# Performance work log

Measured on AMD Instinct MI355X. Metric: run time of the kernel, lower is better.

## Reference

```python
import jax, jax.numpy as jnp
import numpy as np

B, N = 4, 8192
DIM, HEADS = 512, 8
DH = DIM // HEADS
DT, DELTA, FF = 128, 64, 4 * DIM


def _lin(key, fan_in, fan_out):
    # torch nn.Linear default init: U(-1/sqrt(fan_in), 1/sqrt(fan_in))
    s = 1.0 / np.sqrt(fan_in)
    k1, k2 = jax.random.split(key)
    w = jax.random.uniform(k1, (fan_in, fan_out), minval=-s, maxval=s, dtype=jnp.float32)
    b = jax.random.uniform(k2, (fan_out,), minval=-s, maxval=s, dtype=jnp.float32)
    return w, b


def setup_inputs() -> dict:
    key = jax.random.key(0)
    ks = jax.random.split(key, 16)
    inp = {}
    inp['node_features'] = jax.random.normal(ks[0], (B, N, DIM), dtype=jnp.float32)
    inp['diffusion_time'] = jax.random.normal(ks[1], (B, DT), dtype=jnp.float32)
    inp['positions'] = jax.random.normal(ks[2], (B, N, 2), dtype=jnp.float32)
    inp['node_mask'] = jnp.ones((B, N), dtype=jnp.float32)
    inp['yy_w'], inp['yy_b'] = _lin(ks[3], DT, DT)
    inp['pos1_w'], inp['pos1_b'] = _lin(ks[4], 2, 64)
    inp['pos2_w'], inp['pos2_b'] = _lin(ks[5], 64, DELTA)
    inp['linx_w'], inp['linx_b'] = _lin(ks[6], DIM, DIM)
    inp['cat_w'], inp['cat_b'] = _lin(ks[7], DIM + DELTA + DT, DIM)
    inp['ln1_g'] = jnp.ones((DIM,), jnp.float32)
    inp['ln1_b'] = jnp.zeros((DIM,), jnp.float32)
    inp['q_w'] = _lin(ks[8], DIM, DIM)[0]  # no bias
    inp['k_w'] = _lin(ks[9], DIM, DIM)[0]
    inp['v_w'] = _lin(ks[10], DIM, DIM)[0]
    inp['attn_out_w'], inp['attn_out_b'] = _lin(ks[11], DIM, DIM)
    inp['ln2_g'] = jnp.ones((DIM,), jnp.float32)
    inp['ln2_b'] = jnp.zeros((DIM,), jnp.float32)
    inp['ff1_w'], inp['ff1_b'] = _lin(ks[12], DIM, FF)
    inp['ff2_w'], inp['ff2_b'] = _lin(ks[13], FF, DIM)
    inp['head2pos_w'], inp['head2pos_b'] = _lin(ks[14], DIM, 2)
    return inp


def _layernorm(x, g, b, eps=1e-5):
    mu = jnp.mean(x, axis=-1, keepdims=True)
    var = jnp.mean(jnp.square(x - mu), axis=-1, keepdims=True)
    return (x - mu) * jax.lax.rsqrt(var + eps) * g + b


def reference(node_features, diffusion_time, positions, node_mask,
              yy_w, yy_b, pos1_w, pos1_b, pos2_w, pos2_b,
              linx_w, linx_b, cat_w, cat_b,
              ln1_g, ln1_b, q_w, k_w, v_w, attn_out_w, attn_out_b,
              ln2_g, ln2_b, ff1_w, ff1_b, ff2_w, ff2_b,
              head2pos_w, head2pos_b):
    b, n, _ = node_features.shape
    mask = node_mask[..., None]  # (b, n, 1)

    # transform_diffusion_time (not last layer): y = y_y(diffusion_time)
    y = diffusion_time @ yy_w + yy_b  # (b, dy)

    # transform_positions_for_attention
    p = positions * mask
    pnorm = jnp.linalg.norm(p, axis=-1, keepdims=True)
    p_unit = p / (pnorm + 1e-7)
    delta = jax.nn.relu(p_unit @ pos1_w + pos1_b) @ pos2_w + pos2_b  # (b, n, delta)

    # feature concat + projection
    tx = node_features @ linx_w + linx_b  # (b, n, dim)
    t = jnp.broadcast_to(y[:, None, :], (b, n, y.shape[-1]))
    cat = jnp.concatenate([tx, delta, t], axis=-1) @ cat_w + cat_b  # (b, n, dim)

    # LinearAttentionTransformer, depth=1, non-causal global linear attention
    # block 1: x = x + attn(LN(x))
    h = _layernorm(cat, ln1_g, ln1_b)
    q = (h @ q_w).reshape(b, n, HEADS, DH).transpose(0, 2, 1, 3)  # (b, h, n, d)
    k = (h @ k_w).reshape(b, n, HEADS, DH).transpose(0, 2, 1, 3)
    v = (h @ v_w).reshape(b, n, HEADS, DH).transpose(0, 2, 1, 3)
    q = jax.nn.softmax(q, axis=-1) * (DH ** -0.5)  # softmax over feature dim
    k = jax.nn.softmax(k, axis=2)                   # softmax over sequence dim
    context = jnp.einsum('bhnd,bhne->bhde', k, v)   # (b, h, d, d)
    attn = jnp.einsum('bhnd,bhde->bhne', q, context)  # (b, h, n, d)
    attn = attn.transpose(0, 2, 1, 3).reshape(b, n, DIM)
    x = cat + (attn @ attn_out_w + attn_out_b)

    # block 2: x = x + ff(LN(x)), GELU feedforward
    h2 = _layernorm(x, ln2_g, ln2_b)
    x = x + (jax.nn.gelu(h2 @ ff1_w + ff1_b) @ ff2_w + ff2_b)

    # head_features_to_position
    pos_out = x @ head2pos_w + head2pos_b  # (b, n, 2)
    return (x, y, pos_out)
```

## Files before the change

### kernel.cpp

```cpp
#include <hip/hip_runtime.h>
#include <hip/hip_bf16.h>
#include <math.h>

#define NB 4
#define NN 8192
#define ROWS (NB*NN)
#define DIMC 512
#define HEADS 8
#define DT 128
#define DELTA 64
#define FF 2048
#define KCATP 640

#define OFF_R0     ((size_t)0)
#define OFF_CAW    ((size_t)8388608)
#define OFF_R1     ((size_t)10485760)
#define OFF_R2     ((size_t)18874368)
#define OFF_CATWT  ((size_t)27262976)
#define OFF_KVT    ((size_t)27426816)
#define OFF_QWT    ((size_t)27688960)
#define OFF_F1WT   ((size_t)27820032)
#define OFF_F2WT   ((size_t)28344320)
#define OFF_LXWB   ((size_t)28868608)
#define OFF_CW0T   ((size_t)28999680)
#define OFF_Y      ((size_t)29130752)
#define OFF_BB     ((size_t)29131264)
#define OFF_PM     ((size_t)29133312)
#define OFF_PS     ((size_t)29264384)
#define OFF_M      ((size_t)29395456)
#define OFF_SINV   ((size_t)29397504)
#define OFF_CTX    ((size_t)29399552)

typedef __attribute__((ext_vector_type(8))) short bf16x8;
typedef __attribute__((ext_vector_type(4))) float f32x4;
typedef __attribute__((ext_vector_type(8))) unsigned short us8;

static __device__ __forceinline__ unsigned short f2b(float x) {
    __hip_bfloat16 h = __float2bfloat16(x);
    return __builtin_bit_cast(unsigned short, h);
}
static __device__ __forceinline__ float b2f(unsigned short u) {
    return __bfloat162float(__builtin_bit_cast(__hip_bfloat16, u));
}
static __device__ __forceinline__ float gelu_tanh(float x) {
    float z2 = 1.5957691216057308f * (x + 0.044715f * x * x * x);
    float t = __expf(z2);
    return x - x / (t + 1.0f);
}

#define GLOAD16(g, l) __builtin_amdgcn_global_load_lds( \
    (const __attribute__((address_space(1))) void*)(g), \
    (__attribute__((address_space(3))) void*)(l), 16, 0, 0)

__global__ void y_kernel(const float* __restrict__ dt, const float* __restrict__ yyw,
                         const float* __restrict__ yyb, float* __restrict__ y_ws,
                         float* __restrict__ y_out) {
    int idx = blockIdx.x * 128 + threadIdx.x;
    int b = idx >> 7, j = idx & 127;
    float acc = yyb[j];
    for (int c = 0; c < DT; ++c) acc += dt[b * DT + c] * yyw[c * DT + j];
    y_ws[idx] = acc;
    y_out[idx] = acc;
}

__global__ void bb_kernel(const float* __restrict__ linxb, const float* __restrict__ catw,
                          const float* __restrict__ catb, const float* __restrict__ y,
                          float* __restrict__ bb) {
    int idx = blockIdx.x * 256 + threadIdx.x;
    int b = idx >> 9, n = idx & 511;
    float acc = catb[n];
    for (int c = 0; c < DIMC; ++c) acc += linxb[c] * catw[(size_t)c * DIMC + n];
    const float* cw3 = catw + (size_t)(DIMC + DELTA) * DIMC;
    for (int j = 0; j < DT; ++j) acc += y[b * DT + j] * cw3[(size_t)j * DIMC + n];
    bb[idx] = acc;
}

__global__ __launch_bounds__(256) void delta_kernel(
    const float* __restrict__ pos, const float* __restrict__ mask,
    const float* __restrict__ w1, const float* __restrict__ b1,
    const float* __restrict__ w2, const float* __restrict__ b2,
    unsigned short* __restrict__ catA) {
    int lane = threadIdx.x & 63;
    size_t row = (size_t)blockIdx.x * 4 + (threadIdx.x >> 6);
    float mk = mask[row];
    float px = pos[row * 2] * mk, py = pos[row * 2 + 1] * mk;
    float nrm = sqrtf(px * px + py * py) + 1e-7f;
    float ux = px / nrm, uy = py / nrm;
    float t1 = fmaxf(ux * w1[lane] + uy * w1[64 + lane] + b1[lane], 0.0f);
    float acc = b2[lane];
    #pragma unroll
    for (int j = 0; j < 64; ++j) {
        float tv = __shfl(t1, j, 64);
        acc += tv * w2[j * 64 + lane];
    }
    catA[row * KCATP + DIMC + lane] = f2b(acc);
    catA[row * KCATP + 576 + lane] = 0;
}

__global__ void zcat_kernel(unsigned short* __restrict__ catWT) {
    int idx = blockIdx.x * 256 + threadIdx.x;
    int n = idx >> 6, c = 576 + (idx & 63);
    catWT[(size_t)n * KCATP + c] = 0;
}

__global__ void conv_bf16(const float* __restrict__ in, unsigned short* __restrict__ out, int n8) {
    int i = blockIdx.x * 256 + threadIdx.x;
    if (i >= n8) return;
    const float* p = in + (size_t)i * 8;
    us8 o;
    #pragma unroll
    for (int j = 0; j < 8; ++j) o[j] = f2b(p[j]);
    *(us8*)(out + (size_t)i * 8) = o;
}

__global__ void conv_bf16_strided(const float* __restrict__ in, unsigned short* __restrict__ out,
                                  int ldo) {
    int i = blockIdx.x * 256 + threadIdx.x;
    int row = i >> 6, c8 = (i & 63) * 8;
    const float* p = in + (size_t)row * DIMC + c8;
    us8 o;
    #pragma unroll
    for (int j = 0; j < 8; ++j) o[j] = f2b(p[j]);
    *(us8*)(out + (size_t)row * ldo + c8) = o;
}

__global__ __launch_bounds__(256) void transconv(const float* __restrict__ in,
                                                 unsigned short* __restrict__ out,
                                                 int R, int C, int ldo) {
    __shared__ float tile[32][33];
    int bx = blockIdx.x * 32;
    int by = blockIdx.y * 32;
    int tx = threadIdx.x & 31, ty = threadIdx.x >> 5;
    #pragma unroll
    for (int i = 0; i < 4; ++i) {
        int r = ty + i * 8;
        tile[r][tx] = in[(size_t)(by + r) * C + bx + tx];
    }
    __syncthreads();
    #pragma unroll
    for (int i = 0; i < 4; ++i) {
        int r = ty + i * 8;
        out[(size_t)(bx + r) * ldo + by + tx] = f2b(tile[tx][r]);
    }
}

__global__ __launch_bounds__(128) void ln_kernel(
    const float* __restrict__ src, unsigned short* __restrict__ dst,
    const float* __restrict__ g, const float* __restrict__ bta) {
    size_t row = blockIdx.x;
    int t = threadIdx.x;
    const float* s = src + row * DIMC;
    float4 x = *(const float4*)(s + t * 4);
    float sum = x.x + x.y + x.z + x.w;
    float sq = x.x * x.x + x.y * x.y + x.z * x.z + x.w * x.w;
    #pragma unroll
    for (int o = 32; o; o >>= 1) { sum += __shfl_down(sum, o, 64); sq += __shfl_down(sq, o, 64); }
    __shared__ float sh[4];
    if ((t & 63) == 0) { sh[(t >> 6) * 2] = sum; sh[(t >> 6) * 2 + 1] = sq; }
    __syncthreads();
    sum = sh[0] + sh[2]; sq = sh[1] + sh[3];
    float mean = sum * (1.0f / DIMC);
    float var = sq * (1.0f / DIMC) - mean * mean;
    float rstd = rsqrtf(fmaxf(var, 0.0f) + 1e-5f);
    float4 gv = *(const float4*)(g + t * 4);
    float4 bv = *(const float4*)(bta + t * 4);
    ushort4 ov;
    ov.x = f2b((x.x - mean) * rstd * gv.x + bv.x);
    ov.y = f2b((x.y - mean) * rstd * gv.y + bv.y);
    ov.z = f2b((x.z - mean) * rstd * gv.z + bv.z);
    ov.w = f2b((x.w - mean) * rstd * gv.w + bv.w);
    *(ushort4*)(dst + row * DIMC + t * 4) = ov;
}

template <int EPI, int SWZ>
__global__ __launch_bounds__(512, 4) void gemm256(
    const unsigned short* __restrict__ A, int lda,
    const unsigned short* __restrict__ Bt, int ldb,
    const float* __restrict__ bias,
    const float* __restrict__ extra, int batch_rows,
    void* __restrict__ Cv, void* __restrict__ Cv2,
    int M, int N, int K,
    size_t b_stride, int rows_per_batch) {
    extern __shared__ char lds[];
    const int tid = threadIdx.x;
    const int lane = tid & 63, wv = tid >> 6;
    const int wr = wv >> 1, wc = wv & 1;
    const int lr = lane & 15, lch = lane >> 4;

    int bxi = blockIdx.x, byi = blockIdx.y;
    if constexpr (SWZ) {
        int l = byi * gridDim.x + bxi;
        int xcd = l & 7, j = l >> 3;
        byi = xcd * (gridDim.y >> 3) + j / gridDim.x;
        bxi = j % gridDim.x;
    }
    const int bm = byi * 256, bn = bxi * 128;

    const unsigned short* Bb = Bt;
    if (rows_per_batch) Bb = Bt + (size_t)(bm / rows_per_batch) * b_stride;

    const int srow = tid >> 2;
    const int schunk = tid & 3;

    auto stage = [&](int s, int kcol) {
        char* dstA = lds + (size_t)s * 24576;
        #pragma unroll
        for (int i = 0; i < 2; ++i) {
            int row = srow + 128 * i;
            int gc = schunk ^ ((row >> 1) & 3);
            GLOAD16((const char*)(A + (size_t)(bm + row) * lda + kcol) + gc * 16,
                    dstA + (size_t)(tid + 512 * i) * 16);
        }
        char* dstB = lds + (size_t)s * 24576 + 16384;
        {
            int row = srow;
            int gc = schunk ^ ((row >> 1) & 3);
            GLOAD16((const char*)(Bb + (size_t)(bn + row) * ldb + kcol) + gc * 16,
                    dstB + (size_t)tid * 16);
        }
    };

    f32x4 acc[4][4] = {};
    const int nt = K >> 5;

    stage(0, 0);
    stage(1, 32);
    __builtin_amdgcn_sched_barrier(0);
    asm volatile("s_waitcnt vmcnt(3)" ::: "memory");
    __builtin_amdgcn_sched_barrier(0);
    __builtin_amdgcn_s_barrier();

    int slot = 0;
    for (int t = 0; t < nt; ++t) {
        const char* base = lds + (size_t)slot * 24576;
        bf16x8 afr[4], bfr[4];
        #pragma unroll
        for (int n = 0; n < 4; ++n) {
            int bc = wc * 64 + n * 16 + lr;
            bfr[n] = *(const bf16x8*)(base + 16384 + bc * 64 + ((lch ^ ((bc >> 1) & 3)) << 4));
        }
        #pragma unroll
        for (int m = 0; m < 4; ++m) {
            int ar = wr * 64 + m * 16 + lr;
            afr[m] = *(const bf16x8*)(base + ar * 64 + ((lch ^ ((ar >> 1) & 3)) << 4));
        }
        const bool pf2 = (t + 2 < nt);
        if (pf2) {
            int s2 = slot >= 1 ? slot - 1 : 2;
            stage(s2, (t + 2) << 5);
        }
        __builtin_amdgcn_sched_barrier(0);
        asm volatile("s_waitcnt lgkmcnt(0)" ::: "memory");
        __builtin_amdgcn_sched_barrier(0);
        __builtin_amdgcn_s_setprio(1);
        #pragma unroll
        for (int m = 0; m < 4; ++m)
            #pragma unroll
            for (int n = 0; n < 4; ++n)
                acc[m][n] = __builtin_amdgcn_mfma_f32_16x16x32_bf16(
                    afr[m], bfr[n], acc[m][n], 0, 0, 0);
        __builtin_amdgcn_s_setprio(0);
        if (t + 1 < nt) {
            if (pf2) asm volatile("s_waitcnt vmcnt(3)" ::: "memory");
            else     asm volatile("s_waitcnt vmcnt(0)" ::: "memory");
            __builtin_amdgcn_sched_barrier(0);
        }
        __builtin_amdgcn_s_barrier();
        slot = slot < 2 ? slot + 1 : 0;
    }

    const int g4 = lch * 4;
    if constexpr (EPI == 7) {
        #pragma unroll
        for (int m = 0; m < 4; ++m)
            #pragma unroll
            for (int r = 0; r < 4; ++r) {
                float v0 = acc[m][0][r], v1 = acc[m][1][r];
                float v2 = acc[m][2][r], v3 = acc[m][3][r];
                float mx = fmaxf(fmaxf(v0, v1), fmaxf(v2, v3));
                #pragma unroll
                for (int o = 1; o < 16; o <<= 1) mx = fmaxf(mx, __shfl_xor(mx, o, 64));
                float e0 = __expf(v0 - mx), e1 = __expf(v1 - mx);
                float e2 = __expf(v2 - mx), e3 = __expf(v3 - mx);
                float s = e0 + e1 + e2 + e3;
                #pragma unroll
                for (int o = 1; o < 16; o <<= 1) s += __shfl_xor(s, o, 64);
                float sc = 0.125f / s;
                int rr = bm + wr * 64 + m * 16 + g4 + r;
                unsigned short* dst = (unsigned short*)Cv + (size_t)rr * N + bn + wc * 64 + lr;
                dst[0]  = f2b(e0 * sc);
                dst[16] = f2b(e1 * sc);
                dst[32] = f2b(e2 * sc);
                dst[48] = f2b(e3 * sc);
            }
    } else {
        #pragma unroll
        for (int m = 0; m < 4; ++m)
            #pragma unroll
            for (int n = 0; n < 4; ++n) {
                int col = bn + wc * 64 + n * 16 + lr;
                #pragma unroll
                for (int r = 0; r < 4; ++r) {
                    int rr = bm + wr * 64 + m * 16 + g4 + r;
                    float v = acc[m][n][r];
                    if (EPI == 1) {
                        ((unsigned short*)Cv)[(size_t)rr * N + col] = f2b(gelu_tanh(v + bias[col]));
                    } else if (EPI == 2) {
                        ((float*)Cv)[(size_t)rr * N + col] += v + bias[col];
                    } else if (EPI == 3) {
                        ((float*)Cv)[(size_t)rr * N + col] = v + extra[(size_t)(rr / batch_rows) * N + col];
                    } else if (EPI == 6) {
                        unsigned short* dst = (col >> 9) ? (unsigned short*)Cv2 : (unsigned short*)Cv;
                        dst[(size_t)rr * 512 + (col & 511)] = f2b(v);
                    }
                }
            }
    }
}

#define BM 128
#define BN 128
#define BK 64

template <int EPI>
__global__ __launch_bounds__(256) void gemm_mfma(
    const unsigned short* __restrict__ A, int lda,
    const unsigned short* __restrict__ Bt, int ldb,
    void* __restrict__ Cv, int M, int N, int K, int ldo) {
    __shared__ unsigned short As[2][BM * BK];
    __shared__ unsigned short Bs[2][BN * BK];
    int bm = blockIdx.y * BM, bn = blockIdx.x * BN;
    int tid = threadIdx.x;
    int lane = tid & 63, wv = tid >> 6;
    int wr = (wv >> 1) * 64, wc = (wv & 1) * 64;
    int g16 = (lane >> 4) << 4;
    int lr = lane & 15;
    int sw = (lr & 7) << 4;

    int srow = tid >> 3;
    int skb = (tid & 7) * 16;
    int sxor = skb ^ ((srow & 7) << 4);

    auto stage = [&](int buf, int k0) {
        #pragma unroll
        for (int i = 0; i < 4; ++i) {
            int row = srow + 32 * i;
            GLOAD16((const char*)(A + (size_t)(bm + row) * lda + k0) + sxor,
                    (char*)As[buf] + (size_t)(tid + 256 * i) * 16);
        }
        #pragma unroll
        for (int i = 0; i < 4; ++i) {
            int row = srow + 32 * i;
            GLOAD16((const char*)(Bt + (size_t)(bn + row) * ldb + k0) + sxor,
                    (char*)Bs[buf] + (size_t)(tid + 256 * i) * 16);
        }
    };

    f32x4 acc[4][4] = {};
    int nt = K / BK;
    stage(0, 0);
    __syncthreads();
    for (int t = 0; t < nt; ++t) {
        int cur = t & 1;
        if (t + 1 < nt) stage(cur ^ 1, (t + 1) * BK);
        const char* Ab = (const char*)As[cur];
        const char* Bp = (const char*)Bs[cur];
        #pragma unroll
        for (int s = 0; s < 2; ++s) {
            int koff = s * 64 + g16;
            bf16x8 af[4], bw[4];
            #pragma unroll
            for (int f = 0; f < 4; ++f) {
                int ar = wr + f * 16 + lr;
                af[f] = *(const bf16x8*)(Ab + ar * 128 + (koff ^ sw));
                int br = wc + f * 16 + lr;
                bw[f] = *(const bf16x8*)(Bp + br * 128 + (koff ^ sw));
            }
            #pragma unroll
            for (int f = 0; f < 4; ++f)
                #pragma unroll
                for (int j = 0; j < 4; ++j)
                    acc[f][j] = __builtin_amdgcn_mfma_f32_16x16x32_bf16(
                        af[f], bw[j], acc[f][j], 0, 0, 0);
        }
        __syncthreads();
    }

    int g4 = (lane >> 4) * 4;
    #pragma unroll
    for (int f = 0; f < 4; ++f) {
        #pragma unroll
        for (int j = 0; j < 4; ++j) {
            int col = bn + wc + j * 16 + lr;
            #pragma unroll
            for (int r = 0; r < 4; ++r) {
                int rr = bm + wr + f * 16 + g4 + r;
                float v = acc[f][j][r];
                if (EPI == 4) {
                    ((unsigned short*)Cv)[(size_t)rr * N + col] = f2b(v);
                } else if (EPI == 5) {
                    ((unsigned short*)Cv)[(size_t)col * ldo + rr] = f2b(v);
                }
            }
        }
    }
}

__global__ __launch_bounds__(256) void ksm_stats1(
    const unsigned short* __restrict__ k, float* __restrict__ pm, float* __restrict__ ps) {
    int b = blockIdx.y, rb = blockIdx.x;
    const unsigned short* kp = k + ((size_t)b * NN + (size_t)rb * 128) * DIMC;
    int t = threadIdx.x;
    float m0 = -1e30f, s0 = 0.f, m1 = -1e30f, s1 = 0.f;
    for (int r = 0; r < 128; ++r) {
        float x0 = b2f(kp[(size_t)r * DIMC + t]);
        float x1 = b2f(kp[(size_t)r * DIMC + t + 256]);
        float n0 = fmaxf(m0, x0), n1 = fmaxf(m1, x1);
        s0 = s0 * __expf(m0 - n0) + __expf(x0 - n0);
        s1 = s1 * __expf(m1 - n1) + __expf(x1 - n1);
        m0 = n0; m1 = n1;
    }
    size_t base = ((size_t)b * 64 + rb) * DIMC;
    pm[base + t] = m0; pm[base + t + 256] = m1;
    ps[base + t] = s0; ps[base + t + 256] = s1;
}

__global__ void ksm_stats2(const float* __restrict__ pm, const float* __restrict__ ps,
                           float* __restrict__ Mst, float* __restrict__ Sinv) {
    int idx = blockIdx.x * 256 + threadIdx.x;
    int b = idx >> 9, c = idx & 511;
    float m = -1e30f, s = 0.f;
    for (int rb = 0; rb < 64; ++rb) {
        float mm = pm[((size_t)b * 64 + rb) * DIMC + c];
        float ss = ps[((size_t)b * 64 + rb) * DIMC + c];
        if (mm > m) { s = s * __expf(m - mm) + ss; m = mm; } else s += ss * __expf(mm - m);
    }
    Mst[idx] = m;
    Sinv[idx] = 1.f / s;
}

__global__ __launch_bounds__(256) void context_kernel(
    const unsigned short* __restrict__ kb, const unsigned short* __restrict__ vb,
    const float* __restrict__ Mst, const float* __restrict__ Sinv,
    float* __restrict__ ctx) {
    int b = blockIdx.z, hd = blockIdx.y, rb = blockIdx.x;
    int tid = threadIdx.x, tx = tid & 15, ty = tid >> 4;
    __shared__ float kx[64][68];
    __shared__ float vx[64][68];
    int r0t = tid >> 3;
    int c8 = (tid & 7) * 8;
    int cb = hd * 64 + c8;
    float mv[8], sv[8];
    #pragma unroll
    for (int j = 0; j < 8; ++j) { mv[j] = Mst[b * DIMC + cb + j]; sv[j] = Sinv[b * DIMC + cb + j]; }
    float cacc[4][4] = {};
    for (int sub = 0; sub < 8; ++sub) {
        size_t row0 = (size_t)b * NN + (size_t)rb * 512 + sub * 64;
        #pragma unroll
        for (int i = 0; i < 2; ++i) {
            int r = r0t + i * 32;
            us8 kv = *(const us8*)(kb + (row0 + r) * DIMC + cb);
            us8 vv = *(const us8*)(vb + (row0 + r) * DIMC + cb);
            #pragma unroll
            for (int j = 0; j < 8; ++j) {
                kx[r][c8 + j] = __expf(b2f(kv[j]) - mv[j]) * sv[j];
                vx[r][c8 + j] = b2f(vv[j]);
            }
        }
        __syncthreads();
        #pragma unroll 4
        for (int r = 0; r < 64; ++r) {
            float4 a4 = *(const float4*)&kx[r][ty * 4];
            float4 b4 = *(const float4*)&vx[r][tx * 4];
            float av[4] = {a4.x, a4.y, a4.z, a4.w};
            float bv[4] = {b4.x, b4.y, b4.z, b4.w};
            #pragma unroll
            for (int i = 0; i < 4; ++i)
                #pragma unroll
                for (int j = 0; j < 4; ++j)
                    cacc[i][j] = fmaf(av[i], bv[j], cacc[i][j]);
        }
        __syncthreads();
    }
    size_t cbase = (size_t)(b * HEADS + hd) * 64 * 64;
    #pragma unroll
    for (int i = 0; i < 4; ++i)
        #pragma unroll
        for (int j = 0; j < 4; ++j)
            atomicAdd(&ctx[cbase + (size_t)(ty * 4 + i) * 64 + tx * 4 + j], cacc[i][j]);
}

__global__ __launch_bounds__(256) void caw_kernel(const float* __restrict__ ctx,
                                                  const float* __restrict__ aow,
                                                  float* __restrict__ caw) {
    int nt = blockIdx.x, hd = blockIdx.y, b = blockIdx.z;
    int tid = threadIdx.x, tx = tid & 15, ty = tid >> 4;
    __shared__ float cs[64][68];
    __shared__ float aw[64][68];
    #pragma unroll
    for (int i = 0; i < 4; ++i) {
        int idx = tid + 256 * i;
        int r = idx >> 4, c4 = (idx & 15) * 4;
        *(float4*)&cs[r][c4] = *(const float4*)(ctx + ((size_t)(b * HEADS + hd) * 64 + r) * 64 + c4);
        *(float4*)&aw[r][c4] = *(const float4*)(aow + (size_t)(hd * 64 + r) * DIMC + nt * 64 + c4);
    }
    __syncthreads();
    float acc[4][4] = {};
    for (int e = 0; e < 64; ++e) {
        float av[4];
        #pragma unroll
        for (int i = 0; i < 4; ++i) av[i] = cs[ty * 4 + i][e];
        float4 b4 = *(const float4*)&aw[e][tx * 4];
        float bv[4] = {b4.x, b4.y, b4.z, b4.w};
        #pragma unroll
        for (int i = 0; i < 4; ++i)
            #pragma unroll
            for (int j = 0; j < 4; ++j)
                acc[i][j] = fmaf(av[i], bv[j], acc[i][j]);
    }
    #pragma unroll
    for (int i = 0; i < 4; ++i)
        #pragma unroll
        for (int j = 0; j < 4; ++j)
            caw[(size_t)b * DIMC * DIMC + (size_t)(hd * 64 + ty * 4 + i) * DIMC + nt * 64 + tx * 4 + j]
                = acc[i][j];
}

__global__ __launch_bounds__(256) void pos_kernel(
    const float* __restrict__ x, const float* __restrict__ w,
    const float* __restrict__ b2, float* __restrict__ out) {
    int lane = threadIdx.x & 63;
    size_t row = (size_t)blockIdx.x * 4 + (threadIdx.x >> 6);
    const float* xp = x + row * DIMC;
    float acc0 = 0.f, acc1 = 0.f;
    #pragma unroll
    for (int i = 0; i < 2; ++i) {
        float4 xv = *(const float4*)(xp + lane * 8 + i * 4);
        const float* wp = w + (size_t)(lane * 8 + i * 4) * 2;
        float4 w0 = *(const float4*)(wp);
        float4 w1 = *(const float4*)(wp + 4);
        acc0 += xv.x * w0.x + xv.y * w0.z + xv.z * w1.x + xv.w * w1.z;
        acc1 += xv.x * w0.y + xv.y * w0.w + xv.z * w1.y + xv.w * w1.w;
    }
    #pragma unroll
    for (int o = 32; o; o >>= 1) { acc0 += __shfl_down(acc0, o, 64); acc1 += __shfl_down(acc1, o, 64); }
    if (lane == 0) {
        out[row * 2] = acc0 + b2[0];
        out[row * 2 + 1] = acc1 + b2[1];
    }
}

extern "C" void kernel_launch(void* const* d_in, const int* in_sizes, int n_in,
                              void* d_out, int out_size, void* d_ws, size_t ws_size,
                              hipStream_t stream) {
    (void)in_sizes; (void)n_in; (void)out_size; (void)ws_size;
    const float* nf  = (const float*)d_in[0];
    const float* dt  = (const float*)d_in[1];
    const float* pos = (const float*)d_in[2];
    const float* msk = (const float*)d_in[3];
    const float* yyw = (const float*)d_in[4];
    const float* yyb = (const float*)d_in[5];
    const float* p1w = (const float*)d_in[6];
    const float* p1b = (const float*)d_in[7];
    const float* p2w = (const float*)d_in[8];
    const float* p2b = (const float*)d_in[9];
    const float* lxw = (const float*)d_in[10];
    const float* lxb = (const float*)d_in[11];
    const float* cw  = (const float*)d_in[12];
    const float* cb  = (const float*)d_in[13];
    const float* l1g = (const float*)d_in[14];
    const float* l1b = (const float*)d_in[15];
    const float* qw  = (const float*)d_in[16];
    const float* kw  = (const float*)d_in[17];
    const float* vw  = (const float*)d_in[18];
    const float* aow = (const float*)d_in[19];
    const float* aob = (const float*)d_in[20];
    const float* l2g = (const float*)d_in[21];
    const float* l2b = (const float*)d_in[22];
    const float* f1w = (const float*)d_in[23];
    const float* f1b = (const float*)d_in[24];
    const float* f2w = (const float*)d_in[25];
    const float* f2b_ = (const float*)d_in[26];
    const float* hpw = (const float*)d_in[27];
    const float* hpb = (const float*)d_in[28];

    float* ws = (float*)d_ws;
    unsigned short* catA_u  = (unsigned short*)(ws + OFF_R0);
    unsigned short* hb_u    = (unsigned short*)(ws + OFF_R0);
    float*          caw     = ws + OFF_CAW;
    unsigned short* kb_u    = (unsigned short*)(ws + OFF_R1);
    unsigned short* qb_u    = (unsigned short*)(ws + OFF_R1);
    unsigned short* mid_u   = (unsigned short*)(ws + OFF_R1);
    unsigned short* vb_u    = (unsigned short*)(ws + OFF_R2);
    unsigned short* cawT_u  = (unsigned short*)(ws + OFF_R2);
    unsigned short* catWT_u = (unsigned short*)(ws + OFF_CATWT);
    unsigned short* kvT_u   = (unsigned short*)(ws + OFF_KVT);
    unsigned short* qwT_u   = (unsigned short*)(ws + OFF_QWT);
    unsigned short* f1wT_u  = (unsigned short*)(ws + OFF_F1WT);
    unsigned short* f2wT_u  = (unsigned short*)(ws + OFF_F2WT);
    unsigned short* lxwb_u  = (unsigned short*)(ws + OFF_LXWB);
    unsigned short* cw0T_u  = (unsigned short*)(ws + OFF_CW0T);
    float* yv   = ws + OFF_Y;
    float* bbf  = ws + OFF_BB;
    float* pm   = ws + OFF_PM;
    float* ps2  = ws + OFF_PS;
    float* Mst  = ws + OFF_M;
    float* Sinv = ws + OFF_SINV;
    float* ctx  = ws + OFF_CTX;

    float* xout = (float*)d_out;
    float* yout = xout + (size_t)ROWS * DIMC;
    float* pout = yout + NB * DT;

    hipFuncSetAttribute(reinterpret_cast<const void*>(&gemm256<1, 1>),
                        hipFuncAttributeMaxDynamicSharedMemorySize, 73728);
    hipFuncSetAttribute(reinterpret_cast<const void*>(&gemm256<2, 0>),
                        hipFuncAttributeMaxDynamicSharedMemorySize, 73728);
    hipFuncSetAttribute(reinterpret_cast<const void*>(&gemm256<3, 0>),
                        hipFuncAttributeMaxDynamicSharedMemorySize, 73728);
    hipFuncSetAttribute(reinterpret_cast<const void*>(&gemm256<6, 0>),
                        hipFuncAttributeMaxDynamicSharedMemorySize, 73728);
    hipFuncSetAttribute(reinterpret_cast<const void*>(&gemm256<7, 0>),
                        hipFuncAttributeMaxDynamicSharedMemorySize, 73728);

    y_kernel<<<4, 128, 0, stream>>>(dt, yyw, yyb, yv, yout);
    bb_kernel<<<8, 256, 0, stream>>>(lxb, cw, cb, yv, bbf);
    conv_bf16<<<128, 256, 0, stream>>>(lxw, lxwb_u, 32768);
    transconv<<<dim3(16, 16), 256, 0, stream>>>(cw, cw0T_u, 512, 512, 512);
    transconv<<<dim3(16, 2), 256, 0, stream>>>(cw + (size_t)DIMC * DIMC, catWT_u + 512, 64, 512, KCATP);
    zcat_kernel<<<128, 256, 0, stream>>>(catWT_u);
    transconv<<<dim3(16, 16), 256, 0, stream>>>(kw, kvT_u, 512, 512, 512);
    transconv<<<dim3(16, 16), 256, 0, stream>>>(vw, kvT_u + (size_t)512 * 512, 512, 512, 512);
    transconv<<<dim3(16, 16), 256, 0, stream>>>(qw, qwT_u, 512, 512, 512);
    transconv<<<dim3(64, 16), 256, 0, stream>>>(f1w, f1wT_u, 512, 2048, 512);
    transconv<<<dim3(16, 64), 256, 0, stream>>>(f2w, f2wT_u, 2048, 512, 2048);
    conv_bf16_strided<<<8192, 256, 0, stream>>>(nf, catA_u, KCATP);
    delta_kernel<<<8192, 256, 0, stream>>>(pos, msk, p1w, p1b, p2w, p2b, catA_u);

    gemm_mfma<5><<<dim3(4, 4), 256, 0, stream>>>(
        lxwb_u, 512, cw0T_u, 512, catWT_u, 512, 512, 512, KCATP);

    gemm256<3, 0><<<dim3(4, 128), 512, 73728, stream>>>(
        catA_u, KCATP, catWT_u, KCATP, nullptr, bbf, NN,
        xout, nullptr, ROWS, 512, KCATP, 0, 0);

    ln_kernel<<<ROWS, 128, 0, stream>>>(xout, hb_u, l1g, l1b);

    gemm256<6, 0><<<dim3(8, 128), 512, 73728, stream>>>(
        hb_u, 512, kvT_u, 512, nullptr, nullptr, 0,
        kb_u, vb_u, ROWS, 1024, 512, 0, 0);

    ksm_stats1<<<dim3(64, 4), 256, 0, stream>>>(kb_u, pm, ps2);
    ksm_stats2<<<8, 256, 0, stream>>>(pm, ps2, Mst, Sinv);

    hipMemsetAsync(ctx, 0, (size_t)NB * HEADS * 64 * 64 * sizeof(float), stream);
    context_kernel<<<dim3(16, HEADS, NB), 256, 0, stream>>>(kb_u, vb_u, Mst, Sinv, ctx);

    gemm256<7, 0><<<dim3(4, 128), 512, 73728, stream>>>(
        hb_u, 512, qwT_u, 512, nullptr, nullptr, 0,
        qb_u, nullptr, ROWS, 512, 512, 0, 0);

    caw_kernel<<<dim3(8, 8, 4), 256, 0, stream>>>(ctx, aow, caw);
    for (int b = 0; b < NB; ++b)
        transconv<<<dim3(16, 16), 256, 0, stream>>>(caw + (size_t)b * 262144,
                                                    cawT_u + (size_t)b * 262144, 512, 512, 512);

    gemm256<2, 0><<<dim3(4, 128), 512, 73728, stream>>>(
        qb_u, 512, cawT_u, 512, aob, nullptr, 0,
        xout, nullptr, ROWS, 512, 512, 262144, NN);

    ln_kernel<<<ROWS, 128, 0, stream>>>(xout, hb_u, l2g, l2b);
    for (int bp = 0; bp < 2; ++bp) {
        const unsigned short* hbp = hb_u + (size_t)bp * 16384 * DIMC;
        gemm256<1, 1><<<dim3(16, 64), 512, 73728, stream>>>(
            hbp, 512, f1wT_u, 512, f1b, nullptr, 0,
            mid_u, nullptr, 16384, FF, 512, 0, 0);
        gemm256<2, 0><<<dim3(4, 64), 512, 73728, stream>>>(
            mid_u, 2048, f2wT_u, 2048, f2b_, nullptr, 0,
            xout + (size_t)bp * 16384 * DIMC, nullptr, 16384, 512, 2048, 0, 0);
    }

    pos_kernel<<<8192, 256, 0, stream>>>(xout, hpw, hpb, pout);
}
```

Before: 643.2 us.

## Store K/V transposed and compute softmax stats and context with MFMA

The K/V projection GEMM now writes K and V in feature-major (transposed) layout through an LDS staging epilogue. This lets the key softmax statistics be computed by one wave per feature with contiguous reads, replacing the two-pass partial-stats kernels. The context einsum moves from scalar FMA in LDS to bf16 MFMA, with a per-block LDS reduction before the atomics. The second template parameter of several GEMMs is also switched from 0 to 1. The exp-scaled K is rounded to bf16 before the MFMA, which costs some precision.

```diff
diff --git a/kernel.cpp b/kernel.cpp
--- a/kernel.cpp
+++ b/kernel.cpp
@@ -25,8 +25,6 @@
 #define OFF_CW0T   ((size_t)28999680)
 #define OFF_Y      ((size_t)29130752)
 #define OFF_BB     ((size_t)29131264)
-#define OFF_PM     ((size_t)29133312)
-#define OFF_PS     ((size_t)29264384)
 #define OFF_M      ((size_t)29395456)
 #define OFF_SINV   ((size_t)29397504)
 #define OFF_CTX    ((size_t)29399552)
@@ -293,6 +291,33 @@
                 dst[32] = f2b(e2 * sc);
                 dst[48] = f2b(e3 * sc);
             }
+    } else if constexpr (EPI == 8) {
+        unsigned short* tb = (unsigned short*)(lds + (size_t)wv * 8704);
+        #pragma unroll
+        for (int m = 0; m < 4; ++m)
+            #pragma unroll
+            for (int n = 0; n < 4; ++n)
+                #pragma unroll
+                for (int r = 0; r < 4; ++r) {
+                    int row_l = m * 16 + g4 + r;
+                    int col_l = n * 16 + lr;
+                    tb[col_l * 68 + row_l] = f2b(acc[m][n][r]);
+                }
+        asm volatile("s_waitcnt lgkmcnt(0)" ::: "memory");
+        __builtin_amdgcn_sched_barrier(0);
+        #pragma unroll
+        for (int q2 = 0; q2 < 8; ++q2) {
+            int col_l = (lane >> 3) + q2 * 8;
+            int row0 = (lane & 7) * 8;
+            ushort4 lo = *(const ushort4*)(tb + col_l * 68 + row0);
+            ushort4 hi = *(const ushort4*)(tb + col_l * 68 + row0 + 4);
+            int colg = bn + wc * 64 + col_l;
+            int rowg = bm + wr * 64 + row0;
+            unsigned short* dstb = (colg < 512) ? (unsigned short*)Cv : (unsigned short*)Cv2;
+            unsigned short* d = dstb + (size_t)(colg & 511) * ROWS + rowg;
+            *(ushort4*)(d) = lo;
+            *(ushort4*)(d + 4) = hi;
+        }
     } else {
         #pragma unroll
         for (int m = 0; m < 4; ++m)
@@ -406,88 +431,92 @@
     }
 }
 
-__global__ __launch_bounds__(256) void ksm_stats1(
-    const unsigned short* __restrict__ k, float* __restrict__ pm, float* __restrict__ ps) {
-    int b = blockIdx.y, rb = blockIdx.x;
-    const unsigned short* kp = k + ((size_t)b * NN + (size_t)rb * 128) * DIMC;
-    int t = threadIdx.x;
-    float m0 = -1e30f, s0 = 0.f, m1 = -1e30f, s1 = 0.f;
-    for (int r = 0; r < 128; ++r) {
-        float x0 = b2f(kp[(size_t)r * DIMC + t]);
-        float x1 = b2f(kp[(size_t)r * DIMC + t + 256]);
-        float n0 = fmaxf(m0, x0), n1 = fmaxf(m1, x1);
-        s0 = s0 * __expf(m0 - n0) + __expf(x0 - n0);
-        s1 = s1 * __expf(m1 - n1) + __expf(x1 - n1);
-        m0 = n0; m1 = n1;
-    }
-    size_t base = ((size_t)b * 64 + rb) * DIMC;
-    pm[base + t] = m0; pm[base + t + 256] = m1;
-    ps[base + t] = s0; ps[base + t + 256] = s1;
-}
-
-__global__ void ksm_stats2(const float* __restrict__ pm, const float* __restrict__ ps,
-                           float* __restrict__ Mst, float* __restrict__ Sinv) {
-    int idx = blockIdx.x * 256 + threadIdx.x;
-    int b = idx >> 9, c = idx & 511;
+__global__ __launch_bounds__(256) void ksm_rows(
+    const unsigned short* __restrict__ kbT, float* __restrict__ Mst, float* __restrict__ Sinv) {
+    int seg = blockIdx.x * 4 + (threadIdx.x >> 6);
+    int lane = threadIdx.x & 63;
+    int b = seg >> 9, f = seg & 511;
+    const unsigned short* p = kbT + (size_t)f * ROWS + (size_t)b * NN;
     float m = -1e30f, s = 0.f;
-    for (int rb = 0; rb < 64; ++rb) {
-        float mm = pm[((size_t)b * 64 + rb) * DIMC + c];
-        float ss = ps[((size_t)b * 64 + rb) * DIMC + c];
-        if (mm > m) { s = s * __expf(m - mm) + ss; m = mm; } else s += ss * __expf(mm - m);
-    }
-    Mst[idx] = m;
-    Sinv[idx] = 1.f / s;
-}
-
-__global__ __launch_bounds__(256) void context_kernel(
-    const unsigned short* __restrict__ kb, const unsigned short* __restrict__ vb,
+    for (int it = 0; it < 16; ++it) {
+        us8 v = *(const us8*)(p + (size_t)(it * 64 + lane) * 8);
+        #pragma unroll
+        for (int j = 0; j < 8; ++j) {
+            float x = b2f(v[j]);
+            float n = fmaxf(m, x);
+            s = s * __expf(m - n) + __expf(x - n);
+            m = n;
+        }
+    }
+    #pragma unroll
+    for (int o = 1; o < 64; o <<= 1) {
+        float mo = __shfl_xor(m, o, 64), so = __shfl_xor(s, o, 64);
+        float n = fmaxf(m, mo);
+        s = s * __expf(m - n) + so * __expf(mo - n);
+        m = n;
+    }
+    if (lane == 0) { Mst[seg] = m; Sinv[seg] = 1.f / s; }
+}
+
+__global__ __launch_bounds__(256) void context_mfma(
+    const unsigned short* __restrict__ kbT, const unsigned short* __restrict__ vbT,
     const float* __restrict__ Mst, const float* __restrict__ Sinv,
     float* __restrict__ ctx) {
+    __shared__ float cbuf[4096];
     int b = blockIdx.z, hd = blockIdx.y, rb = blockIdx.x;
-    int tid = threadIdx.x, tx = tid & 15, ty = tid >> 4;
-    __shared__ float kx[64][68];
-    __shared__ float vx[64][68];
-    int r0t = tid >> 3;
-    int c8 = (tid & 7) * 8;
-    int cb = hd * 64 + c8;
-    float mv[8], sv[8];
-    #pragma unroll
-    for (int j = 0; j < 8; ++j) { mv[j] = Mst[b * DIMC + cb + j]; sv[j] = Sinv[b * DIMC + cb + j]; }
-    float cacc[4][4] = {};
-    for (int sub = 0; sub < 8; ++sub) {
-        size_t row0 = (size_t)b * NN + (size_t)rb * 512 + sub * 64;
-        #pragma unroll
-        for (int i = 0; i < 2; ++i) {
-            int r = r0t + i * 32;
-            us8 kv = *(const us8*)(kb + (row0 + r) * DIMC + cb);
-            us8 vv = *(const us8*)(vb + (row0 + r) * DIMC + cb);
-            #pragma unroll
-            for (int j = 0; j < 8; ++j) {
-                kx[r][c8 + j] = __expf(b2f(kv[j]) - mv[j]) * sv[j];
-                vx[r][c8 + j] = b2f(vv[j]);
-            }
-        }
-        __syncthreads();
-        #pragma unroll 4
-        for (int r = 0; r < 64; ++r) {
-            float4 a4 = *(const float4*)&kx[r][ty * 4];
-            float4 b4 = *(const float4*)&vx[r][tx * 4];
-            float av[4] = {a4.x, a4.y, a4.z, a4.w};
-            float bv[4] = {b4.x, b4.y, b4.z, b4.w};
+    int w = threadIdx.x >> 6, lane = threadIdx.x & 63;
+    int lr = lane & 15, lch = lane >> 4;
+    size_t nb = (size_t)b * NN + (size_t)rb * 512 + (size_t)w * 128;
+    float mv[4], sv[4];
+    #pragma unroll
+    for (int i = 0; i < 4; ++i) {
+        mv[i] = Mst[b * DIMC + hd * 64 + i * 16 + lr];
+        sv[i] = Sinv[b * DIMC + hd * 64 + i * 16 + lr];
+    }
+    f32x4 acc[4][4] = {};
+    for (int c = 0; c < 4; ++c) {
+        size_t n0 = nb + c * 32 + lch * 8;
+        bf16x8 af[4], bfv[4];
+        #pragma unroll
+        for (int i = 0; i < 4; ++i) {
+            us8 kv = *(const us8*)(kbT + (size_t)(hd * 64 + i * 16 + lr) * ROWS + n0);
+            bf16x8 a;
+            #pragma unroll
+            for (int j = 0; j < 8; ++j)
+                a[j] = (short)f2b(__expf(b2f(kv[j]) - mv[i]) * sv[i]);
+            af[i] = a;
+            us8 vv = *(const us8*)(vbT + (size_t)(hd * 64 + i * 16 + lr) * ROWS + n0);
+            bfv[i] = __builtin_bit_cast(bf16x8, vv);
+        }
+        #pragma unroll
+        for (int i = 0; i < 4; ++i)
+            #pragma unroll
+            for (int j = 0; j < 4; ++j)
+                acc[i][j] = __builtin_amdgcn_mfma_f32_16x16x32_bf16(
+                    af[i], bfv[j], acc[i][j], 0, 0, 0);
+    }
+    for (int w2 = 0; w2 < 4; ++w2) {
+        if (w == w2) {
             #pragma unroll
             for (int i = 0; i < 4; ++i)
                 #pragma unroll
                 for (int j = 0; j < 4; ++j)
-                    cacc[i][j] = fmaf(av[i], bv[j], cacc[i][j]);
+                    #pragma unroll
+                    for (int r = 0; r < 4; ++r) {
+                        int row = i * 16 + lch * 4 + r;
+                        int col = j * 16 + lr;
+                        int idx = row * 64 + col;
+                        cbuf[idx] = (w2 == 0) ? acc[i][j][r] : cbuf[idx] + acc[i][j][r];
+                    }
         }
         __syncthreads();
     }
-    size_t cbase = (size_t)(b * HEADS + hd) * 64 * 64;
-    #pragma unroll
-    for (int i = 0; i < 4; ++i)
-        #pragma unroll
-        for (int j = 0; j < 4; ++j)
-            atomicAdd(&ctx[cbase + (size_t)(ty * 4 + i) * 64 + tx * 4 + j], cacc[i][j]);
+    size_t cbase = (size_t)(b * HEADS + hd) * 4096;
+    #pragma unroll
+    for (int q = 0; q < 16; ++q) {
+        int idx = threadIdx.x * 16 + q;
+        atomicAdd(&ctx[cbase + idx], cbuf[idx]);
+    }
 }
 
 __global__ __launch_bounds__(256) void caw_kernel(const float* __restrict__ ctx,
@@ -588,10 +617,10 @@
     unsigned short* catA_u  = (unsigned short*)(ws + OFF_R0);
     unsigned short* hb_u    = (unsigned short*)(ws + OFF_R0);
     float*          caw     = ws + OFF_CAW;
-    unsigned short* kb_u    = (unsigned short*)(ws + OFF_R1);
+    unsigned short* kbT_u   = (unsigned short*)(ws + OFF_R1);
     unsigned short* qb_u    = (unsigned short*)(ws + OFF_R1);
     unsigned short* mid_u   = (unsigned short*)(ws + OFF_R1);
-    unsigned short* vb_u    = (unsigned short*)(ws + OFF_R2);
+    unsigned short* vbT_u   = (unsigned short*)(ws + OFF_R2);
     unsigned short* cawT_u  = (unsigned short*)(ws + OFF_R2);
     unsigned short* catWT_u = (unsigned short*)(ws + OFF_CATWT);
     unsigned short* kvT_u   = (unsigned short*)(ws + OFF_KVT);
@@ -602,8 +631,6 @@
     unsigned short* cw0T_u  = (unsigned short*)(ws + OFF_CW0T);
     float* yv   = ws + OFF_Y;
     float* bbf  = ws + OFF_BB;
-    float* pm   = ws + OFF_PM;
-    float* ps2  = ws + OFF_PS;
     float* Mst  = ws + OFF_M;
     float* Sinv = ws + OFF_SINV;
     float* ctx  = ws + OFF_CTX;
@@ -614,13 +641,13 @@
 
     hipFuncSetAttribute(reinterpret_cast<const void*>(&gemm256<1, 1>),
                         hipFuncAttributeMaxDynamicSharedMemorySize, 73728);
-    hipFuncSetAttribute(reinterpret_cast<const void*>(&gemm256<2, 0>),
+    hipFuncSetAttribute(reinterpret_cast<const void*>(&gemm256<2, 1>),
                         hipFuncAttributeMaxDynamicSharedMemorySize, 73728);
-    hipFuncSetAttribute(reinterpret_cast<const void*>(&gemm256<3, 0>),
+    hipFuncSetAttribute(reinterpret_cast<const void*>(&gemm256<3, 1>),
                         hipFuncAttributeMaxDynamicSharedMemorySize, 73728);
-    hipFuncSetAttribute(reinterpret_cast<const void*>(&gemm256<6, 0>),
+    hipFuncSetAttribute(reinterpret_cast<const void*>(&gemm256<7, 1>),
                         hipFuncAttributeMaxDynamicSharedMemorySize, 73728);
-    hipFuncSetAttribute(reinterpret_cast<const void*>(&gemm256<7, 0>),
+    hipFuncSetAttribute(reinterpret_cast<const void*>(&gemm256<8, 1>),
                         hipFuncAttributeMaxDynamicSharedMemorySize, 73728);
 
     y_kernel<<<4, 128, 0, stream>>>(dt, yyw, yyb, yv, yout);
@@ -640,23 +667,22 @@
     gemm_mfma<5><<<dim3(4, 4), 256, 0, stream>>>(
         lxwb_u, 512, cw0T_u, 512, catWT_u, 512, 512, 512, KCATP);
 
-    gemm256<3, 0><<<dim3(4, 128), 512, 73728, stream>>>(
+    gemm256<3, 1><<<dim3(4, 128), 512, 73728, stream>>>(
         catA_u, KCATP, catWT_u, KCATP, nullptr, bbf, NN,
         xout, nullptr, ROWS, 512, KCATP, 0, 0);
 
     ln_kernel<<<ROWS, 128, 0, stream>>>(xout, hb_u, l1g, l1b);
 
-    gemm256<6, 0><<<dim3(8, 128), 512, 73728, stream>>>(
+    gemm256<8, 1><<<dim3(8, 128), 512, 73728, stream>>>(
         hb_u, 512, kvT_u, 512, nullptr, nullptr, 0,
-        kb_u, vb_u, ROWS, 1024, 512, 0, 0);
-
-    ksm_stats1<<<dim3(64, 4), 256, 0, stream>>>(kb_u, pm, ps2);
-    ksm_stats2<<<8, 256, 0, stream>>>(pm, ps2, Mst, Sinv);
+        kbT_u, vbT_u, ROWS, 1024, 512, 0, 0);
+
+    ksm_rows<<<512, 256, 0, stream>>>(kbT_u, Mst, Sinv);
 
     hipMemsetAsync(ctx, 0, (size_t)NB * HEADS * 64 * 64 * sizeof(float), stream);
-    context_kernel<<<dim3(16, HEADS, NB), 256, 0, stream>>>(kb_u, vb_u, Mst, Sinv, ctx);
-
-    gemm256<7, 0><<<dim3(4, 128), 512, 73728, stream>>>(
+    context_mfma<<<dim3(16, HEADS, NB), 256, 0, stream>>>(kbT_u, vbT_u, Mst, Sinv, ctx);
+
+    gemm256<7, 1><<<dim3(4, 128), 512, 73728, stream>>>(
         hb_u, 512, qwT_u, 512, nullptr, nullptr, 0,
         qb_u, nullptr, ROWS, 512, 512, 0, 0);
 
@@ -665,7 +691,7 @@
         transconv<<<dim3(16, 16), 256, 0, stream>>>(caw + (size_t)b * 262144,
                                                     cawT_u + (size_t)b * 262144, 512, 512, 512);
 
-    gemm256<2, 0><<<dim3(4, 128), 512, 73728, stream>>>(
+    gemm256<2, 1><<<dim3(4, 128), 512, 73728, stream>>>(
         qb_u, 512, cawT_u, 512, aob, nullptr, 0,
         xout, nullptr, ROWS, 512, 512, 262144, NN);
 
@@ -675,7 +701,7 @@
         gemm256<1, 1><<<dim3(16, 64), 512, 73728, stream>>>(
             hbp, 512, f1wT_u, 512, f1b, nullptr, 0,
             mid_u, nullptr, 16384, FF, 512, 0, 0);
-        gemm256<2, 0><<<dim3(4, 64), 512, 73728, stream>>>(
+        gemm256<2, 1><<<dim3(4, 64), 512, 73728, stream>>>(
             mid_u, 2048, f2wT_u, 2048, f2b_, nullptr, 0,
             xout + (size_t)bp * 16384 * DIMC, nullptr, 16384, 512, 2048, 0, 0);
     }
```

Measured after the change: 636.5 us. About the same (-1.0%).
